# Kernel optimization log

Hardware: AMD Instinct MI355X
Metric: run time of the kernel (lower is better)

Reference implementation:

```python
import jax, jax.numpy as jnp
import numpy as np

HIDDEN = 256
DEPTH = 3
MOL_ATOMS = 42  # padding_final_size in MPNEncoder.padding (AM_dim0=False)
ATOM_FDIM = 133
BOND_FDIM = 147
N_MOLS = 4000
N_ATOMS = N_MOLS * MOL_ATOMS
N_BONDS = 360000
MAX_NB = 6


def setup_inputs() -> dict:
    key = jax.random.key(0)
    ks = jax.random.split(key, 9)
    f_atoms = jax.random.normal(ks[0], (N_ATOMS, ATOM_FDIM), dtype=jnp.float32)
    f_bonds = jax.random.normal(ks[1], (N_BONDS, BOND_FDIM), dtype=jnp.float32)
    a2b = jax.random.randint(ks[2], (N_ATOMS, MAX_NB), 0, N_BONDS, dtype=jnp.int32)
    b2a = jax.random.randint(ks[3], (N_BONDS,), 0, N_ATOMS, dtype=jnp.int32)
    b2revb = jax.random.randint(ks[4], (N_BONDS,), 0, N_BONDS, dtype=jnp.int32)
    # learned params (bias=False for W_i/W_h, W_o has bias, per chemprop defaults)
    W_i = jax.random.normal(ks[5], (HIDDEN, BOND_FDIM), dtype=jnp.float32) * 0.05
    W_h = jax.random.normal(ks[6], (HIDDEN, HIDDEN), dtype=jnp.float32) * 0.05
    W_o = jax.random.normal(ks[7], (HIDDEN, ATOM_FDIM + HIDDEN), dtype=jnp.float32) * 0.05
    b_o = jax.random.normal(ks[8], (HIDDEN,), dtype=jnp.float32) * 0.05
    return dict(f_atoms=f_atoms, f_bonds=f_bonds, W_i=W_i, W_h=W_h, W_o=W_o,
                b_o=b_o, a2b=a2b, b2a=b2a, b2revb=b2revb)


def reference(f_atoms, f_bonds, W_i, W_h, W_o, b_o, a2b, b2a, b2revb):
    # bond-message MPN (atom_messages=False, undirected=False, dropout=0)
    relu = jax.nn.relu
    inp = f_bonds @ W_i.T                         # [n_bonds, H]
    message = relu(inp)

    def atom_hidden(a_msg):
        a_input = jnp.concatenate([f_atoms, a_msg], axis=1)  # [n_atoms, fa+H]
        return relu(a_input @ W_o.T + b_o)

    # depth-0 hidden: a_input = [f_atoms, zeros(H)] (the 'padding' tensor)
    save_depth = [atom_hidden(jnp.zeros((f_atoms.shape[0], HIDDEN), f_atoms.dtype))]
    for d in range(DEPTH - 1):
        if d == 0:
            save_depth.append(atom_hidden(message[a2b].sum(axis=1)))
        a_message = message[a2b].sum(axis=1)      # gather+sum over neighbors
        message = a_message[b2a] - message[b2revb]
        message = relu(inp + message @ W_h.T)
        save_depth.append(atom_hidden(message[a2b].sum(axis=1)))

    # every molecule has exactly MOL_ATOMS atoms -> padding() is identity,
    # per-molecule narrow/stack becomes a reshape
    def pool(h):
        return h.reshape(N_MOLS, MOL_ATOMS, HIDDEN)

    d0, d1, d2 = pool(save_depth[0]), pool(save_depth[1]), pool(save_depth[2])
    dfin = pool(save_depth[-1])
    mol_vecs = dfin.mean(axis=1)                  # sum / a_size
    return (d0, d1, d2, dfin, mol_vecs)
```

## Files before the change

kernel.cpp:

```cpp
#include <hip/hip_runtime.h>

typedef unsigned short u16;
typedef unsigned int u32;
typedef __bf16 bf16x8 __attribute__((ext_vector_type(8)));
typedef float f32x4 __attribute__((ext_vector_type(4)));

__device__ __forceinline__ u16 f2bf(float f) {
  union { float f; u32 u; } c; c.f = f;
  return (u16)((c.u + 0x7fffu + ((c.u >> 16) & 1u)) >> 16);
}
__device__ __forceinline__ float bf2f(u16 h) {
  union { u32 u; float f; } c; c.u = ((u32)h) << 16;
  return c.f;
}
__device__ __forceinline__ float bflo(u32 u) {
  union { u32 u; float f; } c; c.u = u << 16; return c.f;
}
__device__ __forceinline__ float bfhi(u32 u) {
  union { u32 u; float f; } c; c.u = u & 0xffff0000u; return c.f;
}

__global__ __launch_bounds__(256) void cvt_w(const float* __restrict__ src,
                                             u16* __restrict__ dst, int N,
                                             int Ks, int Kd, int src_stride,
                                             int col0) {
  int i = blockIdx.x * 256 + threadIdx.x;
  if (i >= N * Kd) return;
  int n = i / Kd, k = i % Kd;
  float v = (k < Ks) ? src[(size_t)n * src_stride + col0 + k] : 0.f;
  dst[i] = f2bf(v);
}

template <int ASRC, int EPI, int KPAD>
__global__ __launch_bounds__(256, 3) void gemm2(
    const float* __restrict__ Af, int lda, int Kreal,
    const u16* __restrict__ Ab, const u16* __restrict__ Ab2,
    const int* __restrict__ idx1, const int* __restrict__ idx2,
    const u16* __restrict__ Bw,
    const u16* __restrict__ addb, const float* __restrict__ bias,
    u16* __restrict__ outb0, u16* __restrict__ outb1,
    float* __restrict__ outf) {
  constexpr int LDK = KPAD + 8;
  __shared__ u16 As[64 * LDK];

  const int tid = threadIdx.x;
  const int lane = tid & 63, wid = tid >> 6;
  const int wn = wid * 64;
  const int m0 = blockIdx.x * 64;

  if (ASRC == 2) {
    const int r = tid >> 2, part = tid & 3;
    const int gr = m0 + r;
    const int r1 = idx1[gr], r2 = idx2[gr];
    const u16* pa = Ab + (size_t)r1 * KPAD + part * (KPAD / 4);
    const u16* pb = Ab2 + (size_t)r2 * KPAD + part * (KPAD / 4);
    u16* dst = &As[r * LDK + part * (KPAD / 4)];
#pragma unroll
    for (int i = 0; i < KPAD / 32; ++i) {
      uint4 va = *reinterpret_cast<const uint4*>(pa + i * 8);
      uint4 vb = *reinterpret_cast<const uint4*>(pb + i * 8);
      uint4 v;
      u16 t0, t1;
      t0 = f2bf(bflo(va.x) - bflo(vb.x));
      t1 = f2bf(bfhi(va.x) - bfhi(vb.x));
      v.x = (u32)t0 | ((u32)t1 << 16);
      t0 = f2bf(bflo(va.y) - bflo(vb.y));
      t1 = f2bf(bfhi(va.y) - bfhi(vb.y));
      v.y = (u32)t0 | ((u32)t1 << 16);
      t0 = f2bf(bflo(va.z) - bflo(vb.z));
      t1 = f2bf(bfhi(va.z) - bfhi(vb.z));
      v.z = (u32)t0 | ((u32)t1 << 16);
      t0 = f2bf(bflo(va.w) - bflo(vb.w));
      t1 = f2bf(bfhi(va.w) - bfhi(vb.w));
      v.w = (u32)t0 | ((u32)t1 << 16);
      *reinterpret_cast<uint4*>(dst + i * 8) = v;
    }
  } else if (ASRC == 1) {
    constexpr int NCH = 64 * KPAD / 8;
#pragma unroll
    for (int p = 0; p < NCH / 256; ++p) {
      int ch = p * 256 + tid;
      int row = ch / (KPAD / 8);
      int c8 = ch % (KPAD / 8);
      uint4 v = *reinterpret_cast<const uint4*>(Ab + (size_t)m0 * KPAD + (size_t)ch * 8);
      *reinterpret_cast<uint4*>(&As[row * LDK + c8 * 8]) = v;
    }
  } else {
    constexpr int NE = 64 * KPAD;
#pragma unroll
    for (int p = 0; p < NE / 256; ++p) {
      int e = p * 256 + tid;
      int row = e / KPAD, k = e % KPAD;
      float x = (k < Kreal) ? Af[(size_t)(m0 + row) * lda + k] : 0.f;
      As[row * LDK + k] = f2bf(x);
    }
  }
  __syncthreads();

  f32x4 acc[4][4];
#pragma unroll
  for (int i = 0; i < 4; ++i)
#pragma unroll
    for (int j = 0; j < 4; ++j) acc[i][j] = (f32x4)(0.f);

  const int ar = lane & 15, ak = (lane >> 4) * 8;

#pragma unroll
  for (int kk = 0; kk < KPAD; kk += 32) {
    bf16x8 a[4], b[4];
#pragma unroll
    for (int t = 0; t < 4; ++t)
      a[t] = *reinterpret_cast<const bf16x8*>(&As[(t * 16 + ar) * LDK + kk + ak]);
#pragma unroll
    for (int t = 0; t < 4; ++t)
      b[t] = *reinterpret_cast<const bf16x8*>(Bw + (size_t)(wn + t * 16 + ar) * KPAD + kk + ak);
#pragma unroll
    for (int i = 0; i < 4; ++i)
#pragma unroll
      for (int j = 0; j < 4; ++j)
        acc[i][j] = __builtin_amdgcn_mfma_f32_16x16x32_bf16(a[i], b[j], acc[i][j], 0, 0, 0);
  }

  const int er = (lane >> 4) * 4;
  const int ec = lane & 15;
#pragma unroll
  for (int i = 0; i < 4; ++i) {
#pragma unroll
    for (int j = 0; j < 4; ++j) {
      int rbase = m0 + i * 16 + er;
      int c = wn + j * 16 + ec;
#pragma unroll
      for (int q = 0; q < 4; ++q) {
        int r = rbase + q;
        size_t idx = (size_t)r * 256 + c;
        float v = acc[i][j][q];
        if (EPI == 0) {
          outb0[idx] = f2bf(v);
          outb1[idx] = f2bf(v > 0.f ? v : 0.f);
        } else if (EPI == 1) {
          v += bias[c];
          outb0[idx] = f2bf(v);
          outf[idx] = v > 0.f ? v : 0.f;
        } else if (EPI == 2) {
          v += bf2f(addb[idx]);
          outb1[idx] = f2bf(v > 0.f ? v : 0.f);
        } else {
          v += bf2f(addb[idx]);
          outf[idx] = v > 0.f ? v : 0.f;
        }
      }
    }
  }
}

__global__ __launch_bounds__(256) void gather_sum(const u16* __restrict__ msg,
                                                  const int* __restrict__ a2b,
                                                  u16* __restrict__ amsg,
                                                  int n_atoms) {
  int wave = threadIdx.x >> 6, lane = threadIdx.x & 63;
  int atom = blockIdx.x * 4 + wave;
  if (atom >= n_atoms) return;
  float s0 = 0.f, s1 = 0.f, s2 = 0.f, s3 = 0.f;
  int base = atom * 6;
#pragma unroll
  for (int j = 0; j < 6; ++j) {
    int b = a2b[base + j];
    ushort4 v = *reinterpret_cast<const ushort4*>(msg + (size_t)b * 256 + lane * 4);
    s0 += bf2f(v.x);
    s1 += bf2f(v.y);
    s2 += bf2f(v.z);
    s3 += bf2f(v.w);
  }
  ushort4 o = make_ushort4(f2bf(s0), f2bf(s1), f2bf(s2), f2bf(s3));
  *reinterpret_cast<ushort4*>(amsg + (size_t)atom * 256 + lane * 4) = o;
}

__global__ __launch_bounds__(256) void mol_mean(const float* __restrict__ dfin,
                                                float* __restrict__ out) {
  int mol = blockIdx.x, c = threadIdx.x;
  const float* p = dfin + (size_t)mol * (42 * 256) + c;
  float s = 0.f;
#pragma unroll
  for (int a = 0; a < 42; ++a) s += p[a * 256];
  out[(size_t)mol * 256 + c] = s * (1.0f / 42.0f);
}

extern "C" void kernel_launch(void* const* d_in, const int* in_sizes, int n_in,
                              void* d_out, int out_size, void* d_ws,
                              size_t ws_size, hipStream_t stream) {
  const float* f_atoms = (const float*)d_in[0];
  const float* f_bonds = (const float*)d_in[1];
  const float* W_i = (const float*)d_in[2];
  const float* W_h = (const float*)d_in[3];
  const float* W_o = (const float*)d_in[4];
  const float* b_o = (const float*)d_in[5];
  const int* a2b = (const int*)d_in[6];
  const int* b2a = (const int*)d_in[7];
  const int* b2revb = (const int*)d_in[8];

  const int NA = 168000, NB = 360000, H = 256;
  const size_t SZ_BH = (size_t)NB * H * 2;
  const size_t SZ_AH = (size_t)NA * H * 2;

  char* ws = (char*)d_ws;
  u16* inp_b = (u16*)ws;  ws += SZ_BH;
  u16* msgA  = (u16*)ws;  ws += SZ_BH;
  u16* msgB  = (u16*)ws;  ws += SZ_BH;
  u16* amsg  = (u16*)ws;  ws += SZ_AH;
  u16* base_b = (u16*)ws; ws += SZ_AH;
  u16* Wi_b  = (u16*)ws;  ws += 256 * 192 * 2;
  u16* Wh_b  = (u16*)ws;  ws += 256 * 256 * 2;
  u16* Wo1_b = (u16*)ws;  ws += 256 * 192 * 2;
  u16* Wo2_b = (u16*)ws;  ws += 256 * 256 * 2;

  float* out = (float*)d_out;
  float* d0 = out;
  float* d1 = d0 + (size_t)NA * H;
  float* d2 = d1 + (size_t)NA * H;
  float* dfin = d2 + (size_t)NA * H;
  float* mol = dfin + (size_t)NA * H;

  dim3 blk(256);
  cvt_w<<<dim3((256 * 192 + 255) / 256), blk, 0, stream>>>(W_i, Wi_b, 256, 147, 192, 147, 0);
  cvt_w<<<dim3((256 * 256 + 255) / 256), blk, 0, stream>>>(W_h, Wh_b, 256, 256, 256, 256, 0);
  cvt_w<<<dim3((256 * 192 + 255) / 256), blk, 0, stream>>>(W_o, Wo1_b, 256, 133, 192, 389, 0);
  cvt_w<<<dim3((256 * 256 + 255) / 256), blk, 0, stream>>>(W_o, Wo2_b, 256, 256, 256, 389, 133);

  dim3 gB(NB / 64);
  dim3 gA(NA / 64);

  gemm2<0, 0, 192><<<gB, blk, 0, stream>>>(f_bonds, 147, 147, nullptr, nullptr,
                                           nullptr, nullptr, Wi_b, nullptr,
                                           nullptr, inp_b, msgA, nullptr);
  gemm2<0, 1, 192><<<gA, blk, 0, stream>>>(f_atoms, 133, 133, nullptr, nullptr,
                                           nullptr, nullptr, Wo1_b, nullptr,
                                           b_o, base_b, nullptr, d0);

  u16* mcur = msgA;
  u16* mnext = msgB;
  float* douts[3] = {d1, d2, dfin};
  for (int d = 0; d < 3; ++d) {
    gather_sum<<<dim3(NA / 4), blk, 0, stream>>>(mcur, a2b, amsg, NA);
    gemm2<1, 3, 256><<<gA, blk, 0, stream>>>(nullptr, 0, 0, amsg, nullptr,
                                             nullptr, nullptr, Wo2_b, base_b,
                                             nullptr, nullptr, nullptr, douts[d]);
    if (d < 2) {
      gemm2<2, 2, 256><<<gB, blk, 0, stream>>>(nullptr, 0, 0, amsg, mcur, b2a,
                                               b2revb, Wh_b, inp_b, nullptr,
                                               nullptr, mnext, nullptr);
      u16* t = mcur; mcur = mnext; mnext = t;
    }
  }
  mol_mean<<<dim3(4000), blk, 0, stream>>>(dfin, mol);
}
```

Baseline: 1.755 ms.

## Make GEMMs persistent with double-buffered A tiles and register prefetch

Replaces the one-tile-per-block GEMM with a persistent kernel on a fixed grid. Each block walks 32-row tiles, prefetching the next tile's A rows (including the gathered b2a/b2revb rows) into registers while it runs MFMAs on the current LDS buffer. Tile height is halved from 64 to 32 rows and occupancy is raised to 4 blocks per CU. Bias loads are hoisted out of the loop and bf16 packing now uses hardware conversion. The cost is smaller per-tile reuse of the B weights, which are still read from global memory for every tile.

```diff
diff --git a/kernel.cpp b/kernel.cpp
--- a/kernel.cpp
+++ b/kernel.cpp
@@ -5,19 +5,21 @@
 typedef __bf16 bf16x8 __attribute__((ext_vector_type(8)));
 typedef float f32x4 __attribute__((ext_vector_type(4)));
 
-__device__ __forceinline__ u16 f2bf(float f) {
-  union { float f; u32 u; } c; c.f = f;
-  return (u16)((c.u + 0x7fffu + ((c.u >> 16) & 1u)) >> 16);
-}
 __device__ __forceinline__ float bf2f(u16 h) {
-  union { u32 u; float f; } c; c.u = ((u32)h) << 16;
-  return c.f;
+  union { u32 u; float f; } c; c.u = ((u32)h) << 16; return c.f;
 }
 __device__ __forceinline__ float bflo(u32 u) {
   union { u32 u; float f; } c; c.u = u << 16; return c.f;
 }
 __device__ __forceinline__ float bfhi(u32 u) {
   union { u32 u; float f; } c; c.u = u & 0xffff0000u; return c.f;
+}
+__device__ __forceinline__ u32 pack2bf(float a, float b) {
+  union { __bf16 h[2]; u32 u; } c; c.h[0] = (__bf16)a; c.h[1] = (__bf16)b;
+  return c.u;
+}
+__device__ __forceinline__ u16 f2bf(float f) {
+  union { __bf16 h; u16 u; } c; c.h = (__bf16)f; return c.u;
 }
 
 __global__ __launch_bounds__(256) void cvt_w(const float* __restrict__ src,
@@ -32,124 +34,164 @@
 }
 
 template <int ASRC, int EPI, int KPAD>
-__global__ __launch_bounds__(256, 3) void gemm2(
+__global__ __launch_bounds__(256, 4) void gemm3(
     const float* __restrict__ Af, int lda, int Kreal,
     const u16* __restrict__ Ab, const u16* __restrict__ Ab2,
     const int* __restrict__ idx1, const int* __restrict__ idx2,
     const u16* __restrict__ Bw,
     const u16* __restrict__ addb, const float* __restrict__ bias,
     u16* __restrict__ outb0, u16* __restrict__ outb1,
-    float* __restrict__ outf) {
+    float* __restrict__ outf, int ntiles) {
   constexpr int LDK = KPAD + 8;
-  __shared__ u16 As[64 * LDK];
+  __shared__ u16 As[2][32 * LDK];
 
   const int tid = threadIdx.x;
   const int lane = tid & 63, wid = tid >> 6;
   const int wn = wid * 64;
-  const int m0 = blockIdx.x * 64;
-
-  if (ASRC == 2) {
-    const int r = tid >> 2, part = tid & 3;
-    const int gr = m0 + r;
-    const int r1 = idx1[gr], r2 = idx2[gr];
-    const u16* pa = Ab + (size_t)r1 * KPAD + part * (KPAD / 4);
-    const u16* pb = Ab2 + (size_t)r2 * KPAD + part * (KPAD / 4);
-    u16* dst = &As[r * LDK + part * (KPAD / 4)];
-#pragma unroll
-    for (int i = 0; i < KPAD / 32; ++i) {
-      uint4 va = *reinterpret_cast<const uint4*>(pa + i * 8);
-      uint4 vb = *reinterpret_cast<const uint4*>(pb + i * 8);
-      uint4 v;
-      u16 t0, t1;
-      t0 = f2bf(bflo(va.x) - bflo(vb.x));
-      t1 = f2bf(bfhi(va.x) - bfhi(vb.x));
-      v.x = (u32)t0 | ((u32)t1 << 16);
-      t0 = f2bf(bflo(va.y) - bflo(vb.y));
-      t1 = f2bf(bfhi(va.y) - bfhi(vb.y));
-      v.y = (u32)t0 | ((u32)t1 << 16);
-      t0 = f2bf(bflo(va.z) - bflo(vb.z));
-      t1 = f2bf(bfhi(va.z) - bfhi(vb.z));
-      v.z = (u32)t0 | ((u32)t1 << 16);
-      t0 = f2bf(bflo(va.w) - bflo(vb.w));
-      t1 = f2bf(bfhi(va.w) - bfhi(vb.w));
-      v.w = (u32)t0 | ((u32)t1 << 16);
-      *reinterpret_cast<uint4*>(dst + i * 8) = v;
-    }
-  } else if (ASRC == 1) {
-    constexpr int NCH = 64 * KPAD / 8;
-#pragma unroll
-    for (int p = 0; p < NCH / 256; ++p) {
-      int ch = p * 256 + tid;
-      int row = ch / (KPAD / 8);
-      int c8 = ch % (KPAD / 8);
-      uint4 v = *reinterpret_cast<const uint4*>(Ab + (size_t)m0 * KPAD + (size_t)ch * 8);
-      *reinterpret_cast<uint4*>(&As[row * LDK + c8 * 8]) = v;
-    }
-  } else {
-    constexpr int NE = 64 * KPAD;
-#pragma unroll
-    for (int p = 0; p < NE / 256; ++p) {
-      int e = p * 256 + tid;
-      int row = e / KPAD, k = e % KPAD;
-      float x = (k < Kreal) ? Af[(size_t)(m0 + row) * lda + k] : 0.f;
-      As[row * LDK + k] = f2bf(x);
-    }
+  const int stride = gridDim.x;
+
+  float sf[ASRC == 0 ? KPAD / 8 : 1];
+  uint4 sva[ASRC >= 1 ? KPAD / 64 : 1];
+  uint4 svb[ASRC == 2 ? KPAD / 64 : 1];
+
+  auto ISSUE = [&](int t) {
+    int m0 = t * 32;
+    if constexpr (ASRC == 0) {
+#pragma unroll
+      for (int p = 0; p < KPAD / 16; ++p) {
+        int pi = p * 256 + tid;
+        int row = pi / (KPAD / 2), kp = pi % (KPAD / 2);
+        int k0 = kp * 2;
+        const float* src = Af + (size_t)(m0 + row) * lda;
+        sf[2 * p] = (k0 < Kreal) ? src[k0] : 0.f;
+        sf[2 * p + 1] = (k0 + 1 < Kreal) ? src[k0 + 1] : 0.f;
+      }
+    } else if constexpr (ASRC == 1) {
+#pragma unroll
+      for (int p = 0; p < KPAD / 64; ++p) {
+        int ch = p * 256 + tid;
+        sva[p] = *reinterpret_cast<const uint4*>(Ab + (size_t)m0 * KPAD + (size_t)ch * 8);
+      }
+    } else {
+      int row = tid >> 3, part = tid & 7;
+      int gr = m0 + row;
+      int r1 = idx1[gr], r2 = idx2[gr];
+      const u16* pa = Ab + (size_t)r1 * KPAD + part * (KPAD / 8);
+      const u16* pb = Ab2 + (size_t)r2 * KPAD + part * (KPAD / 8);
+#pragma unroll
+      for (int p = 0; p < KPAD / 64; ++p) {
+        sva[p] = *reinterpret_cast<const uint4*>(pa + p * 8);
+        svb[p] = *reinterpret_cast<const uint4*>(pb + p * 8);
+      }
+    }
+  };
+
+  auto WRITE = [&](int buf) {
+    u16* dst = As[buf];
+    if constexpr (ASRC == 0) {
+#pragma unroll
+      for (int p = 0; p < KPAD / 16; ++p) {
+        int pi = p * 256 + tid;
+        int row = pi / (KPAD / 2), kp = pi % (KPAD / 2);
+        *reinterpret_cast<u32*>(&dst[row * LDK + kp * 2]) =
+            pack2bf(sf[2 * p], sf[2 * p + 1]);
+      }
+    } else if constexpr (ASRC == 1) {
+#pragma unroll
+      for (int p = 0; p < KPAD / 64; ++p) {
+        int ch = p * 256 + tid;
+        int row = ch / (KPAD / 8), c8 = ch % (KPAD / 8);
+        *reinterpret_cast<uint4*>(&dst[row * LDK + c8 * 8]) = sva[p];
+      }
+    } else {
+      int row = tid >> 3, part = tid & 7;
+#pragma unroll
+      for (int p = 0; p < KPAD / 64; ++p) {
+        uint4 va = sva[p], vb = svb[p], v;
+        v.x = pack2bf(bflo(va.x) - bflo(vb.x), bfhi(va.x) - bfhi(vb.x));
+        v.y = pack2bf(bflo(va.y) - bflo(vb.y), bfhi(va.y) - bfhi(vb.y));
+        v.z = pack2bf(bflo(va.z) - bflo(vb.z), bfhi(va.z) - bfhi(vb.z));
+        v.w = pack2bf(bflo(va.w) - bflo(vb.w), bfhi(va.w) - bfhi(vb.w));
+        *reinterpret_cast<uint4*>(&dst[row * LDK + part * (KPAD / 8) + p * 8]) = v;
+      }
+    }
+  };
+
+  f32x4 acc[2][4];
+  const int ar = lane & 15, ak = (lane >> 4) * 8;
+  const int er = (lane >> 4) * 4, ec = lane & 15;
+
+  float bv[4];
+  if constexpr (EPI == 1) {
+#pragma unroll
+    for (int j = 0; j < 4; ++j) bv[j] = bias[wn + j * 16 + ec];
   }
+
+  int tile = blockIdx.x;
+  ISSUE(tile);
+  WRITE(0);
   __syncthreads();
-
-  f32x4 acc[4][4];
-#pragma unroll
-  for (int i = 0; i < 4; ++i)
-#pragma unroll
-    for (int j = 0; j < 4; ++j) acc[i][j] = (f32x4)(0.f);
-
-  const int ar = lane & 15, ak = (lane >> 4) * 8;
-
-#pragma unroll
-  for (int kk = 0; kk < KPAD; kk += 32) {
-    bf16x8 a[4], b[4];
-#pragma unroll
-    for (int t = 0; t < 4; ++t)
-      a[t] = *reinterpret_cast<const bf16x8*>(&As[(t * 16 + ar) * LDK + kk + ak]);
-#pragma unroll
-    for (int t = 0; t < 4; ++t)
-      b[t] = *reinterpret_cast<const bf16x8*>(Bw + (size_t)(wn + t * 16 + ar) * KPAD + kk + ak);
-#pragma unroll
-    for (int i = 0; i < 4; ++i)
-#pragma unroll
-      for (int j = 0; j < 4; ++j)
-        acc[i][j] = __builtin_amdgcn_mfma_f32_16x16x32_bf16(a[i], b[j], acc[i][j], 0, 0, 0);
-  }
-
-  const int er = (lane >> 4) * 4;
-  const int ec = lane & 15;
-#pragma unroll
-  for (int i = 0; i < 4; ++i) {
-#pragma unroll
-    for (int j = 0; j < 4; ++j) {
-      int rbase = m0 + i * 16 + er;
-      int c = wn + j * 16 + ec;
-#pragma unroll
-      for (int q = 0; q < 4; ++q) {
-        int r = rbase + q;
-        size_t idx = (size_t)r * 256 + c;
-        float v = acc[i][j][q];
-        if (EPI == 0) {
-          outb0[idx] = f2bf(v);
-          outb1[idx] = f2bf(v > 0.f ? v : 0.f);
-        } else if (EPI == 1) {
-          v += bias[c];
-          outb0[idx] = f2bf(v);
-          outf[idx] = v > 0.f ? v : 0.f;
-        } else if (EPI == 2) {
-          v += bf2f(addb[idx]);
-          outb1[idx] = f2bf(v > 0.f ? v : 0.f);
-        } else {
-          v += bf2f(addb[idx]);
-          outf[idx] = v > 0.f ? v : 0.f;
+  int cur = 0;
+
+  while (true) {
+    int nxt = tile + stride;
+    bool hn = nxt < ntiles;
+    if (hn) ISSUE(nxt);
+
+#pragma unroll
+    for (int i = 0; i < 2; ++i)
+#pragma unroll
+      for (int j = 0; j < 4; ++j) acc[i][j] = (f32x4)(0.f);
+
+    const u16* asb = As[cur];
+#pragma unroll
+    for (int kk = 0; kk < KPAD; kk += 32) {
+      bf16x8 a0 = *reinterpret_cast<const bf16x8*>(&asb[ar * LDK + kk + ak]);
+      bf16x8 a1 = *reinterpret_cast<const bf16x8*>(&asb[(16 + ar) * LDK + kk + ak]);
+#pragma unroll
+      for (int j = 0; j < 4; ++j) {
+        bf16x8 b = *reinterpret_cast<const bf16x8*>(
+            Bw + (size_t)(wn + j * 16 + ar) * KPAD + kk + ak);
+        acc[0][j] = __builtin_amdgcn_mfma_f32_16x16x32_bf16(a0, b, acc[0][j], 0, 0, 0);
+        acc[1][j] = __builtin_amdgcn_mfma_f32_16x16x32_bf16(a1, b, acc[1][j], 0, 0, 0);
+      }
+    }
+
+    if (hn) WRITE(cur ^ 1);
+
+    int m0 = tile * 32;
+#pragma unroll
+    for (int i = 0; i < 2; ++i) {
+#pragma unroll
+      for (int j = 0; j < 4; ++j) {
+        int c = wn + j * 16 + ec;
+#pragma unroll
+        for (int q = 0; q < 4; ++q) {
+          int r = m0 + i * 16 + er + q;
+          size_t idx = (size_t)r * 256 + c;
+          float v = acc[i][j][q];
+          if (EPI == 0) {
+            outb0[idx] = f2bf(v);
+            outb1[idx] = f2bf(v > 0.f ? v : 0.f);
+          } else if (EPI == 1) {
+            v += bv[j];
+            outb0[idx] = f2bf(v);
+            outf[idx] = v > 0.f ? v : 0.f;
+          } else if (EPI == 2) {
+            v += bf2f(addb[idx]);
+            outb1[idx] = f2bf(v > 0.f ? v : 0.f);
+          } else {
+            v += bf2f(addb[idx]);
+            outf[idx] = v > 0.f ? v : 0.f;
+          }
         }
       }
     }
+
+    if (!hn) break;
+    __syncthreads();
+    tile = nxt;
+    cur ^= 1;
   }
 }
 
@@ -171,8 +213,10 @@
     s2 += bf2f(v.z);
     s3 += bf2f(v.w);
   }
-  ushort4 o = make_ushort4(f2bf(s0), f2bf(s1), f2bf(s2), f2bf(s3));
-  *reinterpret_cast<ushort4*>(amsg + (size_t)atom * 256 + lane * 4) = o;
+  uint2 o;
+  o.x = pack2bf(s0, s1);
+  o.y = pack2bf(s2, s3);
+  *reinterpret_cast<uint2*>(amsg + (size_t)atom * 256 + lane * 4) = o;
 }
 
 __global__ __launch_bounds__(256) void mol_mean(const float* __restrict__ dfin,
@@ -226,28 +270,29 @@
   cvt_w<<<dim3((256 * 192 + 255) / 256), blk, 0, stream>>>(W_o, Wo1_b, 256, 133, 192, 389, 0);
   cvt_w<<<dim3((256 * 256 + 255) / 256), blk, 0, stream>>>(W_o, Wo2_b, 256, 256, 256, 389, 133);
 
-  dim3 gB(NB / 64);
-  dim3 gA(NA / 64);
-
-  gemm2<0, 0, 192><<<gB, blk, 0, stream>>>(f_bonds, 147, 147, nullptr, nullptr,
-                                           nullptr, nullptr, Wi_b, nullptr,
-                                           nullptr, inp_b, msgA, nullptr);
-  gemm2<0, 1, 192><<<gA, blk, 0, stream>>>(f_atoms, 133, 133, nullptr, nullptr,
-                                           nullptr, nullptr, Wo1_b, nullptr,
-                                           b_o, base_b, nullptr, d0);
+  const int GRID = 1024;
+  int ntB = NB / 32;
+  int ntA = NA / 32;
+
+  gemm3<0, 0, 192><<<dim3(GRID), blk, 0, stream>>>(
+      f_bonds, 147, 147, nullptr, nullptr, nullptr, nullptr, Wi_b, nullptr,
+      nullptr, inp_b, msgA, nullptr, ntB);
+  gemm3<0, 1, 192><<<dim3(GRID), blk, 0, stream>>>(
+      f_atoms, 133, 133, nullptr, nullptr, nullptr, nullptr, Wo1_b, nullptr,
+      b_o, base_b, nullptr, d0, ntA);
 
   u16* mcur = msgA;
   u16* mnext = msgB;
   float* douts[3] = {d1, d2, dfin};
   for (int d = 0; d < 3; ++d) {
     gather_sum<<<dim3(NA / 4), blk, 0, stream>>>(mcur, a2b, amsg, NA);
-    gemm2<1, 3, 256><<<gA, blk, 0, stream>>>(nullptr, 0, 0, amsg, nullptr,
-                                             nullptr, nullptr, Wo2_b, base_b,
-                                             nullptr, nullptr, nullptr, douts[d]);
+    gemm3<1, 3, 256><<<dim3(GRID), blk, 0, stream>>>(
+        nullptr, 0, 0, amsg, nullptr, nullptr, nullptr, Wo2_b, base_b, nullptr,
+        nullptr, nullptr, douts[d], ntA);
     if (d < 2) {
-      gemm2<2, 2, 256><<<gB, blk, 0, stream>>>(nullptr, 0, 0, amsg, mcur, b2a,
-                                               b2revb, Wh_b, inp_b, nullptr,
-                                               nullptr, mnext, nullptr);
+      gemm3<2, 2, 256><<<dim3(GRID), blk, 0, stream>>>(
+          nullptr, 0, 0, amsg, mcur, b2a, b2revb, Wh_b, inp_b, nullptr, nullptr,
+          mnext, nullptr, ntB);
       u16* t = mcur; mcur = mnext; mnext = t;
     }
   }
```

New measurement: 2.483 ms. 1.41x slower.
